# Optimization experiments

Measured on AMD Instinct MI355X. Metric: run time of the kernel, lower is better.

## Reference

```python
import jax, jax.numpy as jnp
import numpy as np

B, S, D = 4, 2048, 1024
H, DK = 16, 64           # n_heads, d_kv; inner_dim = H*DK = 1024 = D
R = 16
SCALING = 32.0 / R       # lora_alpha / r = 2.0


def setup_inputs() -> dict:
    key = jax.random.key(0)
    ks = jax.random.split(key, 10)
    inner = H * DK
    sd = 1.0 / np.sqrt(D)
    return {
        "hidden_states": jax.random.normal(ks[0], (B, S, D), jnp.float32),
        "position_bias": jax.random.normal(ks[1], (1, H, S, S), jnp.float32),
        "Wq": jax.random.normal(ks[2], (inner, D), jnp.float32) * sd,
        "Wk": jax.random.normal(ks[3], (inner, D), jnp.float32) * sd,
        "Wv": jax.random.normal(ks[4], (inner, D), jnp.float32) * sd,
        "Wo": jax.random.normal(ks[5], (D, inner), jnp.float32) * sd,
        "Aq": jax.random.normal(ks[6], (R, D), jnp.float32) * sd,
        "Bq": jax.random.normal(ks[7], (inner, R), jnp.float32) * 0.01,
        "Av": jax.random.normal(ks[8], (R, D), jnp.float32) * sd,
        "Bv": jax.random.normal(ks[9], (inner, R), jnp.float32) * 0.01,
    }


def reference(hidden_states, position_bias, Wq, Wk, Wv, Wo, Aq, Bq, Av, Bv):
    x = hidden_states  # [B,S,D]

    def lora(w_a, w_b):
        # ((x @ A^T) @ B^T) * scaling; low-rank path, rank R
        return ((x @ w_a.T) @ w_b.T) * SCALING

    def heads(t):  # [B,S,H*DK] -> [B,H,S,DK]
        return t.reshape(B, S, H, DK).transpose(0, 2, 1, 3)

    q = heads(x @ Wq.T + lora(Aq, Bq))
    k = heads(x @ Wk.T)
    v = heads(x @ Wv.T + lora(Av, Bv))

    # T5-style: no 1/sqrt(d) scaling; additive position bias
    scores = jnp.einsum("bhqd,bhkd->bhqk", q, k) + position_bias
    attn = jax.nn.softmax(scores, axis=-1)
    out = jnp.einsum("bhqk,bhkd->bhqd", attn, v)
    out = out.transpose(0, 2, 1, 3).reshape(B, S, H * DK)
    return out @ Wo.T
```

## Files before the change

### kernel.cpp

```cpp
#include <hip/hip_runtime.h>
#include <hip/hip_bf16.h>

typedef __bf16 bf16x8 __attribute__((ext_vector_type(8)));
typedef float  f32x4  __attribute__((ext_vector_type(4)));
typedef unsigned short u16;
typedef unsigned long long u64;

#define L2E 1.44269504089f

__device__ __forceinline__ u16 f2b(float f) {
    __bf16 h = (__bf16)f;
    return __builtin_bit_cast(u16, h);
}

typedef const __attribute__((address_space(1))) void* gas1_t;
typedef __attribute__((address_space(3))) void* las3_t;

__device__ __forceinline__ void gl_lds16(const void* g, void* l) {
    __builtin_amdgcn_global_load_lds((gas1_t)g, (las3_t)l, 16, 0, 0);
}


__global__ void cvt_bf16(const float* __restrict__ in, u16* __restrict__ out, int n4) {
    int i = blockIdx.x * 256 + threadIdx.x;
    if (i < n4) {
        float4 v = ((const float4*)in)[i];
        u64 pk = (u64)f2b(v.x) | ((u64)f2b(v.y) << 16) | ((u64)f2b(v.z) << 32) | ((u64)f2b(v.w) << 48);
        ((u64*)out)[i] = pk;
    }
}

__global__ void prep_wqkv(const float* __restrict__ Wq, const float* __restrict__ Wk,
                          const float* __restrict__ Wv, const float* __restrict__ Aq,
                          const float* __restrict__ Bq, const float* __restrict__ Av,
                          const float* __restrict__ Bv, u16* __restrict__ out) {
    int idx = blockIdx.x * 256 + threadIdx.x;
    int n = idx >> 10, j = idx & 1023;
    float v;
    if (n < 1024) {
        v = Wq[n * 1024 + j];
        const float* Br = Bq + n * 16;
        float s = 0.f;
#pragma unroll
        for (int r = 0; r < 16; ++r) s += Br[r] * Aq[r * 1024 + j];
        v += 2.0f * s;
    } else if (n < 2048) {
        v = Wk[(n - 1024) * 1024 + j];
    } else {
        int nn = n - 2048;
        v = Wv[nn * 1024 + j];
        const float* Br = Bv + nn * 16;
        float s = 0.f;
#pragma unroll
        for (int r = 0; r < 16; ++r) s += Br[r] * Av[r * 1024 + j];
        v += 2.0f * s;
    }
    out[idx] = f2b(v);
}


template <int EPI>
__global__ __launch_bounds__(256, 2)
void gemm_bt(const u16* __restrict__ A, const u16* __restrict__ W,
             float* __restrict__ Cout,
             u16* __restrict__ qo, u16* __restrict__ ko, u16* __restrict__ vo,
             int M, int N, int K) {
    __shared__ u16 ldsA[128 * 32];
    __shared__ u16 ldsW[128 * 32];
    const int t = threadIdx.x;
    const int l = t & 63;
    const int m0 = blockIdx.y * 128;
    const int n0 = blockIdx.x * 128;
    const int wm = (t >> 6) >> 1, wn = (t >> 6) & 1;
    const int lc = l & 15, lg = l >> 4;

    const int srow = t >> 2;
    const int sby = ((t & 3) * 16) ^ ((srow & 3) << 4);
    const size_t Ar0 = (size_t)(m0 + srow) * K, Ar1 = (size_t)(m0 + srow + 64) * K;
    const size_t Wr0 = (size_t)(n0 + srow) * K, Wr1 = (size_t)(n0 + srow + 64) * K;
    char* dA = (char*)ldsA;
    char* dW = (char*)ldsW;
    const int d0 = srow * 64 + (t & 3) * 16;
    const int d1 = d0 + 4096;

    f32x4 acc[4][4];
#pragma unroll
    for (int i = 0; i < 4; ++i)
#pragma unroll
        for (int j = 0; j < 4; ++j) acc[i][j] = (f32x4)0.f;

    for (int kt = 0; kt < K; kt += 32) {
        const size_t kb = (size_t)kt * 2;
        gl_lds16((const char*)A + Ar0 * 2 + kb + sby, dA + d0);
        gl_lds16((const char*)A + Ar1 * 2 + kb + sby, dA + d1);
        gl_lds16((const char*)W + Wr0 * 2 + kb + sby, dW + d0);
        gl_lds16((const char*)W + Wr1 * 2 + kb + sby, dW + d1);
        __syncthreads();
        bf16x8 af[4], wf[4];
#pragma unroll
        for (int mi = 0; mi < 4; ++mi) {
            int row = wm * 64 + mi * 16 + lc;
            af[mi] = *(const bf16x8*)(dA + row * 64 + ((lg * 16) ^ ((row & 3) << 4)));
        }
#pragma unroll
        for (int ni = 0; ni < 4; ++ni) {
            int row = wn * 64 + ni * 16 + lc;
            wf[ni] = *(const bf16x8*)(dW + row * 64 + ((lg * 16) ^ ((row & 3) << 4)));
        }
#pragma unroll
        for (int mi = 0; mi < 4; ++mi)
#pragma unroll
            for (int ni = 0; ni < 4; ++ni)
                acc[mi][ni] = __builtin_amdgcn_mfma_f32_16x16x32_bf16(af[mi], wf[ni], acc[mi][ni], 0, 0, 0);
        __syncthreads();
    }

    if (EPI == 0) {
#pragma unroll
        for (int mi = 0; mi < 4; ++mi) {
            int row = m0 + wm * 64 + mi * 16 + lg * 4;
#pragma unroll
            for (int ni = 0; ni < 4; ++ni) {
                int col = n0 + wn * 64 + ni * 16 + lc;
#pragma unroll
                for (int r = 0; r < 4; ++r)
                    Cout[(size_t)(row + r) * N + col] = acc[mi][ni][r];
            }
        }
    } else {
#pragma unroll
        for (int mi = 0; mi < 4; ++mi) {
#pragma unroll
            for (int ni = 0; ni < 4; ++ni) {
                int n = n0 + wn * 64 + ni * 16 + lc;
                int which = n >> 10, inner = n & 1023;
                int h = inner >> 6, dk = inner & 63;
#pragma unroll
                for (int r = 0; r < 4; ++r) {
                    int mrow = m0 + wm * 64 + mi * 16 + lg * 4 + r;
                    int b = mrow >> 11, s = mrow & 2047;
                    size_t bh = (size_t)(b * 16 + h);
                    u16 v = f2b(acc[mi][ni][r]);
                    if (which == 0)      qo[(bh * 2048 + s) * 64 + dk] = v;
                    else if (which == 1) ko[(bh * 2048 + s) * 64 + dk] = v;
                    else                 vo[(bh * 64 + dk) * 2048 + s] = v;
                }
            }
        }
    }
}


__global__ __launch_bounds__(256, 2)
void attn(const u16* __restrict__ Qg, const u16* __restrict__ Kg,
          const u16* __restrict__ Vg, const float* __restrict__ bias,
          u16* __restrict__ Og) {
    __shared__ u16 Kb[2][4096];
    __shared__ u16 Vb[2][4096];
    __shared__ u16 pbuf[4][2048];
    const int t = threadIdx.x;
    const int l = t & 63;
    const int w = t >> 6;
    const int bid = blockIdx.x;
    const int h = bid & 15, b = (bid >> 4) & 3, qt = bid >> 6;
    const int q0 = qt * 128 + w * 32;
    const int lc = l & 15, lg = l >> 4;
    const int rkey = (lc & 7) << 4;
    const size_t bh = (size_t)b * 16 + h;
    const u16* Qp = Qg + bh * 2048 * 64;
    const char* Kpb = (const char*)(Kg + bh * 2048 * 64);
    const char* Vpb = (const char*)(Vg + bh * 64 * 2048);
    char* pb = (char*)pbuf[w];

    const int row0 = w * 8 + (l >> 3);
    const int row1 = row0 + 32;
    const int scol2 = ((l & 7) * 16) ^ (((l >> 3) & 7) << 4);
    const int ldst = w * 1024 + l * 16;

    gl_lds16(Kpb + (size_t)row0 * 128 + scol2, (char*)Kb[0] + ldst);
    gl_lds16(Kpb + (size_t)row1 * 128 + scol2, (char*)Kb[0] + 4096 + ldst);
    gl_lds16(Vpb + (size_t)row0 * 4096 + scol2, (char*)Vb[0] + ldst);
    gl_lds16(Vpb + (size_t)row1 * 4096 + scol2, (char*)Vb[0] + 4096 + ldst);
    asm volatile("" ::: "memory");

    bf16x8 qf[2][2];
#pragma unroll
    for (int mi = 0; mi < 2; ++mi)
#pragma unroll
        for (int ks = 0; ks < 2; ++ks)
            qf[mi][ks] = *(const bf16x8*)&Qp[(size_t)(q0 + mi * 16 + lc) * 64 + ks * 32 + lg * 8];

    f32x4 acc[2][4];
    f32x4 lsum4[2];
#pragma unroll
    for (int mi = 0; mi < 2; ++mi) {
#pragma unroll
        for (int j = 0; j < 4; ++j) acc[mi][j] = (f32x4)0.f;
        lsum4[mi] = (f32x4)0.f;
    }

    const float* bp0 = bias + ((size_t)h * 2048 + q0 + lc) * 2048 + lg * 4;
    float4 br[2][4];
#pragma unroll
    for (int mi = 0; mi < 2; ++mi)
#pragma unroll
        for (int ni = 0; ni < 4; ++ni)
            br[mi][ni] = *(const float4*)(bp0 + (size_t)mi * 16 * 2048 + ni * 16);

    asm volatile("s_waitcnt vmcnt(8)\n\ts_barrier" ::: "memory");

    for (int kt = 0; kt < 32; ++kt) {
        const int cur = kt & 1;
        const int k0 = kt * 64;

        if (kt < 31) {
            const size_t kb = (size_t)(k0 + 64);
            gl_lds16(Kpb + (kb + row0) * 128 + scol2, (char*)Kb[cur ^ 1] + ldst);
            gl_lds16(Kpb + (kb + row1) * 128 + scol2, (char*)Kb[cur ^ 1] + 4096 + ldst);
            gl_lds16(Vpb + (size_t)row0 * 4096 + kb * 2 + scol2, (char*)Vb[cur ^ 1] + ldst);
            gl_lds16(Vpb + (size_t)row1 * 4096 + kb * 2 + scol2, (char*)Vb[cur ^ 1] + 4096 + ldst);
        }
        asm volatile("" ::: "memory");

        f32x4 sfr[4][2];
#pragma unroll
        for (int ni = 0; ni < 4; ++ni)
#pragma unroll
            for (int mi = 0; mi < 2; ++mi) sfr[ni][mi] = (f32x4)0.f;
#pragma unroll
        for (int ks = 0; ks < 2; ++ks) {
            bf16x8 kf[4];
#pragma unroll
            for (int ni = 0; ni < 4; ++ni)
                kf[ni] = *(const bf16x8*)((const char*)Kb[cur] + (ni * 16 + lc) * 128 + ((ks * 64 + lg * 16) ^ rkey));
            __builtin_amdgcn_s_setprio(1);
#pragma unroll
            for (int ni = 0; ni < 4; ++ni)
#pragma unroll
                for (int mi = 0; mi < 2; ++mi)
                    sfr[ni][mi] = __builtin_amdgcn_mfma_f32_16x16x32_bf16(kf[ni], qf[mi][ks], sfr[ni][mi], 0, 0, 0);
            __builtin_amdgcn_s_setprio(0);
        }

#pragma unroll
        for (int mi = 0; mi < 2; ++mi) {
            char* prb = pb + (mi * 16 + lc) * 128;
#pragma unroll
            for (int ni = 0; ni < 4; ++ni) {
                u16 hh[4];
                f32x4 pv;
#pragma unroll
                for (int r = 0; r < 4; ++r) {
                    float p = __builtin_amdgcn_exp2f((sfr[ni][mi][r] + (&br[mi][ni].x)[r]) * L2E);
                    pv[r] = p;
                    hh[r] = f2b(p);
                }
                lsum4[mi] += pv;
                u64 pk = (u64)hh[0] | ((u64)hh[1] << 16) | ((u64)hh[2] << 32) | ((u64)hh[3] << 48);
                *(u64*)(prb + ((ni * 32 + lg * 8) ^ rkey)) = pk;
            }
        }

        if (kt < 31) {
#pragma unroll
            for (int mi = 0; mi < 2; ++mi)
#pragma unroll
                for (int ni = 0; ni < 4; ++ni)
                    br[mi][ni] = *(const float4*)(bp0 + (size_t)mi * 16 * 2048 + k0 + 64 + ni * 16);
        }

#pragma unroll
        for (int ks = 0; ks < 2; ++ks) {
            bf16x8 pf[2], vf[4];
#pragma unroll
            for (int mi = 0; mi < 2; ++mi)
                pf[mi] = *(const bf16x8*)(pb + (mi * 16 + lc) * 128 + ((ks * 64 + lg * 16) ^ rkey));
#pragma unroll
            for (int oni = 0; oni < 4; ++oni)
                vf[oni] = *(const bf16x8*)((const char*)Vb[cur] + (oni * 16 + lc) * 128 + ((ks * 64 + lg * 16) ^ rkey));
            __builtin_amdgcn_s_setprio(1);
#pragma unroll
            for (int mi = 0; mi < 2; ++mi)
#pragma unroll
                for (int oni = 0; oni < 4; ++oni)
                    acc[mi][oni] = __builtin_amdgcn_mfma_f32_16x16x32_bf16(pf[mi], vf[oni], acc[mi][oni], 0, 0, 0);
            __builtin_amdgcn_s_setprio(0);
        }

        asm volatile("s_waitcnt vmcnt(8)\n\ts_barrier" ::: "memory");
    }

    float lsum[2];
#pragma unroll
    for (int mi = 0; mi < 2; ++mi) {
        lsum[mi] = (lsum4[mi][0] + lsum4[mi][1]) + (lsum4[mi][2] + lsum4[mi][3]);
        lsum[mi] += __shfl_xor(lsum[mi], 16);
        lsum[mi] += __shfl_xor(lsum[mi], 32);
    }

#pragma unroll
    for (int mi = 0; mi < 2; ++mi) {
#pragma unroll
        for (int r = 0; r < 4; ++r) {
            int s = q0 + mi * 16 + lg * 4 + r;
            float inv = 1.0f / __shfl(lsum[mi], lg * 4 + r);
            size_t base = ((size_t)b * 2048 + s) * 1024 + h * 64;
#pragma unroll
            for (int oni = 0; oni < 4; ++oni)
                Og[base + oni * 16 + lc] = f2b(acc[mi][oni][r] * inv);
        }
    }
}


extern "C" void kernel_launch(void* const* d_in, const int* in_sizes, int n_in,
                              void* d_out, int out_size, void* d_ws, size_t ws_size,
                              hipStream_t stream) {
    const float* x    = (const float*)d_in[0];
    const float* bias = (const float*)d_in[1];
    const float* Wq   = (const float*)d_in[2];
    const float* Wk   = (const float*)d_in[3];
    const float* Wv   = (const float*)d_in[4];
    const float* Wo   = (const float*)d_in[5];
    const float* Aq   = (const float*)d_in[6];
    const float* Bq   = (const float*)d_in[7];
    const float* Av   = (const float*)d_in[8];
    const float* Bv   = (const float*)d_in[9];
    float* out = (float*)d_out;

    char* ws = (char*)d_ws;
    u16* xb   = (u16*)(ws);
    u16* wqkv = (u16*)(ws + (16ull << 20));
    u16* wob  = (u16*)(ws + (22ull << 20));
    u16* qw   = (u16*)(ws + (24ull << 20));
    u16* kw   = (u16*)(ws + (40ull << 20));
    u16* vw   = (u16*)(ws + (56ull << 20));

    cvt_bf16<<<8192, 256, 0, stream>>>(x, xb, 2097152);
    cvt_bf16<<<1024, 256, 0, stream>>>(Wo, wob, 262144);
    prep_wqkv<<<12288, 256, 0, stream>>>(Wq, Wk, Wv, Aq, Bq, Av, Bv, wqkv);
    gemm_bt<1><<<dim3(24, 64), 256, 0, stream>>>(xb, wqkv, nullptr, qw, kw, vw, 8192, 3072, 1024);
    attn<<<1024, 256, 0, stream>>>(qw, kw, vw, bias, xb);
    gemm_bt<0><<<dim3(8, 64), 256, 0, stream>>>(xb, wob, out, nullptr, nullptr, nullptr, 8192, 1024, 1024);
}
```

Before: 328.5 us.

## Switch attention to 32x32x16 MFMA with register-resident P via permlane32 swap

```diff
diff --git a/kernel.cpp b/kernel.cpp
--- a/kernel.cpp
+++ b/kernel.cpp
@@ -3,7 +3,11 @@
 
 typedef __bf16 bf16x8 __attribute__((ext_vector_type(8)));
 typedef float  f32x4  __attribute__((ext_vector_type(4)));
+typedef float  f32x16 __attribute__((ext_vector_type(16)));
+typedef unsigned u32x2 __attribute__((ext_vector_type(2)));
+typedef unsigned u32x4 __attribute__((ext_vector_type(4)));
 typedef unsigned short u16;
+typedef unsigned u32;
 typedef unsigned long long u64;
 
 #define L2E 1.44269504089f
@@ -151,26 +155,24 @@
 }
 
 
-__global__ __launch_bounds__(256, 2)
+__global__ __launch_bounds__(256, 4)
 void attn(const u16* __restrict__ Qg, const u16* __restrict__ Kg,
           const u16* __restrict__ Vg, const float* __restrict__ bias,
           u16* __restrict__ Og) {
     __shared__ u16 Kb[2][4096];
     __shared__ u16 Vb[2][4096];
-    __shared__ u16 pbuf[4][2048];
     const int t = threadIdx.x;
     const int l = t & 63;
     const int w = t >> 6;
     const int bid = blockIdx.x;
     const int h = bid & 15, b = (bid >> 4) & 3, qt = bid >> 6;
     const int q0 = qt * 128 + w * 32;
-    const int lc = l & 15, lg = l >> 4;
-    const int rkey = (lc & 7) << 4;
+    const int l31 = l & 31, L5 = l >> 5;
+    const int rkey = (l & 7) << 4;
     const size_t bh = (size_t)b * 16 + h;
     const u16* Qp = Qg + bh * 2048 * 64;
     const char* Kpb = (const char*)(Kg + bh * 2048 * 64);
     const char* Vpb = (const char*)(Vg + bh * 64 * 2048);
-    char* pb = (char*)pbuf[w];
 
     const int row0 = w * 8 + (l >> 3);
     const int row1 = row0 + 32;
@@ -183,29 +185,23 @@
     gl_lds16(Vpb + (size_t)row1 * 4096 + scol2, (char*)Vb[0] + 4096 + ldst);
     asm volatile("" ::: "memory");
 
-    bf16x8 qf[2][2];
-#pragma unroll
-    for (int mi = 0; mi < 2; ++mi)
-#pragma unroll
-        for (int ks = 0; ks < 2; ++ks)
-            qf[mi][ks] = *(const bf16x8*)&Qp[(size_t)(q0 + mi * 16 + lc) * 64 + ks * 32 + lg * 8];
-
-    f32x4 acc[2][4];
-    f32x4 lsum4[2];
-#pragma unroll
-    for (int mi = 0; mi < 2; ++mi) {
-#pragma unroll
-        for (int j = 0; j < 4; ++j) acc[mi][j] = (f32x4)0.f;
-        lsum4[mi] = (f32x4)0.f;
-    }
-
-    const float* bp0 = bias + ((size_t)h * 2048 + q0 + lc) * 2048 + lg * 4;
+    bf16x8 qf[4];
+#pragma unroll
+    for (int d = 0; d < 4; ++d)
+        qf[d] = *(const bf16x8*)&Qp[(size_t)(q0 + l31) * 64 + d * 16 + L5 * 8];
+
+    f32x16 acc[2];
+#pragma unroll
+    for (int o = 0; o < 2; ++o) acc[o] = (f32x16)0.f;
+    f32x4 lsum4 = (f32x4)0.f;
+
+    const float* bp0 = bias + ((size_t)h * 2048 + q0 + l31) * 2048 + 4 * L5;
     float4 br[2][4];
 #pragma unroll
-    for (int mi = 0; mi < 2; ++mi)
-#pragma unroll
-        for (int ni = 0; ni < 4; ++ni)
-            br[mi][ni] = *(const float4*)(bp0 + (size_t)mi * 16 * 2048 + ni * 16);
+    for (int ni = 0; ni < 2; ++ni)
+#pragma unroll
+        for (int blk = 0; blk < 4; ++blk)
+            br[ni][blk] = *(const float4*)(bp0 + ni * 32 + blk * 8);
 
     asm volatile("s_waitcnt vmcnt(8)\n\ts_barrier" ::: "memory");
 
@@ -222,94 +218,89 @@
         }
         asm volatile("" ::: "memory");
 
-        f32x4 sfr[4][2];
-#pragma unroll
-        for (int ni = 0; ni < 4; ++ni)
-#pragma unroll
-            for (int mi = 0; mi < 2; ++mi) sfr[ni][mi] = (f32x4)0.f;
-#pragma unroll
-        for (int ks = 0; ks < 2; ++ks) {
+        f32x16 sfr[2];
+#pragma unroll
+        for (int ni = 0; ni < 2; ++ni) {
             bf16x8 kf[4];
 #pragma unroll
-            for (int ni = 0; ni < 4; ++ni)
-                kf[ni] = *(const bf16x8*)((const char*)Kb[cur] + (ni * 16 + lc) * 128 + ((ks * 64 + lg * 16) ^ rkey));
+            for (int d = 0; d < 4; ++d)
+                kf[d] = *(const bf16x8*)((const char*)Kb[cur] + (ni * 32 + l31) * 128 + ((d * 32 + L5 * 16) ^ rkey));
             __builtin_amdgcn_s_setprio(1);
-#pragma unroll
-            for (int ni = 0; ni < 4; ++ni)
-#pragma unroll
-                for (int mi = 0; mi < 2; ++mi)
-                    sfr[ni][mi] = __builtin_amdgcn_mfma_f32_16x16x32_bf16(kf[ni], qf[mi][ks], sfr[ni][mi], 0, 0, 0);
+            sfr[ni] = __builtin_amdgcn_mfma_f32_32x32x16_bf16(kf[0], qf[0], (f32x16)0.f, 0, 0, 0);
+#pragma unroll
+            for (int d = 1; d < 4; ++d)
+                sfr[ni] = __builtin_amdgcn_mfma_f32_32x32x16_bf16(kf[d], qf[d], sfr[ni], 0, 0, 0);
             __builtin_amdgcn_s_setprio(0);
         }
 
-#pragma unroll
-        for (int mi = 0; mi < 2; ++mi) {
-            char* prb = pb + (mi * 16 + lc) * 128;
-#pragma unroll
-            for (int ni = 0; ni < 4; ++ni) {
-                u16 hh[4];
+        u32 Dv[2][4][2];
+#pragma unroll
+        for (int ni = 0; ni < 2; ++ni)
+#pragma unroll
+            for (int blk = 0; blk < 4; ++blk) {
                 f32x4 pv;
 #pragma unroll
-                for (int r = 0; r < 4; ++r) {
-                    float p = __builtin_amdgcn_exp2f((sfr[ni][mi][r] + (&br[mi][ni].x)[r]) * L2E);
-                    pv[r] = p;
-                    hh[r] = f2b(p);
+                for (int off = 0; off < 4; ++off)
+                    pv[off] = __builtin_amdgcn_exp2f((sfr[ni][blk * 4 + off] + (&br[ni][blk].x)[off]) * L2E);
+                lsum4 += pv;
+                asm("v_cvt_pk_bf16_f32 %0, %1, %2" : "=v"(Dv[ni][blk][0]) : "v"(pv[0]), "v"(pv[1]));
+                asm("v_cvt_pk_bf16_f32 %0, %1, %2" : "=v"(Dv[ni][blk][1]) : "v"(pv[2]), "v"(pv[3]));
+            }
+
+        u32x4 pw[4];
+#pragma unroll
+        for (int ni = 0; ni < 2; ++ni)
+#pragma unroll
+            for (int ke = 0; ke < 2; ++ke)
+#pragma unroll
+                for (int c = 0; c < 2; ++c) {
+                    u32x2 r = __builtin_amdgcn_permlane32_swap(Dv[ni][2 * ke][c], Dv[ni][2 * ke + 1][c], false, false);
+                    pw[ni * 2 + ke][c] = r[0];
+                    pw[ni * 2 + ke][2 + c] = r[1];
                 }
-                lsum4[mi] += pv;
-                u64 pk = (u64)hh[0] | ((u64)hh[1] << 16) | ((u64)hh[2] << 32) | ((u64)hh[3] << 48);
-                *(u64*)(prb + ((ni * 32 + lg * 8) ^ rkey)) = pk;
-            }
-        }
+        bf16x8 pf[4];
+#pragma unroll
+        for (int ks = 0; ks < 4; ++ks) pf[ks] = __builtin_bit_cast(bf16x8, pw[ks]);
 
         if (kt < 31) {
 #pragma unroll
-            for (int mi = 0; mi < 2; ++mi)
-#pragma unroll
-                for (int ni = 0; ni < 4; ++ni)
-                    br[mi][ni] = *(const float4*)(bp0 + (size_t)mi * 16 * 2048 + k0 + 64 + ni * 16);
-        }
-
-#pragma unroll
-        for (int ks = 0; ks < 2; ++ks) {
-            bf16x8 pf[2], vf[4];
-#pragma unroll
-            for (int mi = 0; mi < 2; ++mi)
-                pf[mi] = *(const bf16x8*)(pb + (mi * 16 + lc) * 128 + ((ks * 64 + lg * 16) ^ rkey));
-#pragma unroll
-            for (int oni = 0; oni < 4; ++oni)
-                vf[oni] = *(const bf16x8*)((const char*)Vb[cur] + (oni * 16 + lc) * 128 + ((ks * 64 + lg * 16) ^ rkey));
+            for (int ni = 0; ni < 2; ++ni)
+#pragma unroll
+                for (int blk = 0; blk < 4; ++blk)
+                    br[ni][blk] = *(const float4*)(bp0 + k0 + 64 + ni * 32 + blk * 8);
+        }
+
+#pragma unroll
+        for (int o = 0; o < 2; ++o) {
+            bf16x8 vf[4];
+#pragma unroll
+            for (int ks = 0; ks < 4; ++ks)
+                vf[ks] = *(const bf16x8*)((const char*)Vb[cur] + (o * 32 + l31) * 128 + ((ks * 32 + L5 * 16) ^ rkey));
             __builtin_amdgcn_s_setprio(1);
 #pragma unroll
-            for (int mi = 0; mi < 2; ++mi)
-#pragma unroll
-                for (int oni = 0; oni < 4; ++oni)
-                    acc[mi][oni] = __builtin_amdgcn_mfma_f32_16x16x32_bf16(pf[mi], vf[oni], acc[mi][oni], 0, 0, 0);
+            for (int ks = 0; ks < 4; ++ks)
+                acc[o] = __builtin_amdgcn_mfma_f32_32x32x16_bf16(pf[ks], vf[ks], acc[o], 0, 0, 0);
             __builtin_amdgcn_s_setprio(0);
         }
 
         asm volatile("s_waitcnt vmcnt(8)\n\ts_barrier" ::: "memory");
     }
 
-    float lsum[2];
-#pragma unroll
-    for (int mi = 0; mi < 2; ++mi) {
-        lsum[mi] = (lsum4[mi][0] + lsum4[mi][1]) + (lsum4[mi][2] + lsum4[mi][3]);
-        lsum[mi] += __shfl_xor(lsum[mi], 16);
-        lsum[mi] += __shfl_xor(lsum[mi], 32);
-    }
-
-#pragma unroll
-    for (int mi = 0; mi < 2; ++mi) {
-#pragma unroll
-        for (int r = 0; r < 4; ++r) {
-            int s = q0 + mi * 16 + lg * 4 + r;
-            float inv = 1.0f / __shfl(lsum[mi], lg * 4 + r);
-            size_t base = ((size_t)b * 2048 + s) * 1024 + h * 64;
-#pragma unroll
-            for (int oni = 0; oni < 4; ++oni)
-                Og[base + oni * 16 + lc] = f2b(acc[mi][oni][r] * inv);
-        }
-    }
+    float ls = (lsum4[0] + lsum4[1]) + (lsum4[2] + lsum4[3]);
+    ls += __shfl_xor(ls, 32);
+    float inv = 1.0f / ls;
+    float invr[16];
+#pragma unroll
+    for (int r = 0; r < 16; ++r)
+        invr[r] = __shfl(inv, (r & 3) + 8 * (r >> 2) + 4 * L5);
+
+#pragma unroll
+    for (int o = 0; o < 2; ++o)
+#pragma unroll
+        for (int r = 0; r < 16; ++r) {
+            int rowr = (r & 3) + 8 * (r >> 2) + 4 * L5;
+            Og[((size_t)b * 2048 + q0 + rowr) * 1024 + h * 64 + o * 32 + l31] = f2b(acc[o][r] * invr[r]);
+        }
 }
 
 
```

After: 463.9 us. 1.41x slower.
